# Kernel optimization log

Hardware: AMD Instinct MI355X
Metric: run time of the kernel (lower is better)

The kernel has to match this reference:

```python
import jax, jax.numpy as jnp
import numpy as np

N, F, H, OUT, DDIM, E = 200000, 64, 256, 16, 768, 3200000


def setup_inputs() -> dict:
    key = jax.random.key(0)
    ks = jax.random.split(key, 20)
    s = lambda i, shp, sc=0.05: (jax.random.normal(ks[i], shp, jnp.float32) * sc)
    return dict(
        x=jax.random.normal(ks[0], (N, F), jnp.float32),
        edge_index=jax.random.randint(ks[1], (2, E), 0, N, dtype=jnp.int32),
        doc_feature=jax.random.normal(ks[2], (DDIM,), jnp.float32),
        pool_w=s(3, (F,)),
        init_weight=s(4, (F, F)),
        gru_w_ih=s(5, (3 * F, F)), gru_w_hh=s(6, (3 * F, F)),
        gru_b_ih=s(7, (3 * F,)), gru_b_hh=s(8, (3 * F,)),
        gnn_fc_w=s(9, (H, F)), gnn_fc_b=s(10, (H,)),
        doc_fc_w=s(11, (H, DDIM)), doc_fc_b=s(12, (H,)),
        ln_g=jnp.ones((2 * H,), jnp.float32), ln_b=jnp.zeros((2 * H,), jnp.float32),
        fusion_w=s(13, (H, 2 * H)), fusion_b=s(14, (H,)),
        task_w=s(15, (OUT, H)), task_b=s(16, (OUT,)),
        time_w=s(17, (1, H)), time_b=s(18, (1,)),
    )


def _forward(x, doc_feature, pool_w, init_weight, gru_w_ih, gru_w_hh, gru_b_ih,
             gru_b_hh, gnn_fc_w, gnn_fc_b, doc_fc_w, doc_fc_b, ln_g, ln_b,
             fusion_w, fusion_b, task_w, task_b, time_w, time_b, edge_index):
    n, f = x.shape
    # --- EvolveGCNH: TopK pooling, k = f since ratio = in_channels/num_nodes ---
    score = x @ pool_w / jnp.linalg.norm(pool_w)             # [n]
    top_s, perm = jax.lax.top_k(score, f)
    x_tilde = x[perm] * jnp.tanh(top_s)[:, None]             # [f, f]
    # --- single-step GRU; hidden state = previous GCN weight (detached) ---
    h0 = jax.lax.stop_gradient(init_weight)                  # [f, f]
    gx = x_tilde @ gru_w_ih.T + gru_b_ih                     # [f, 3f]
    gh = h0 @ gru_w_hh.T + gru_b_hh
    xr, xz, xn = jnp.split(gx, 3, axis=1)
    hr, hz, hn = jnp.split(gh, 3, axis=1)
    r = jax.nn.sigmoid(xr + hr)
    z = jax.nn.sigmoid(xz + hz)
    nc = jnp.tanh(xn + r * hn)
    W = (1.0 - z) * nc + z * h0                              # evolved weight [f, f]
    # --- GCNConv with fixed W: sym-norm adjacency with self loops ---
    xw = x @ W                                               # [n, f]
    loop = jnp.arange(n, dtype=edge_index.dtype)
    row = jnp.concatenate([edge_index[0], loop])
    col = jnp.concatenate([edge_index[1], loop])
    deg = jax.ops.segment_sum(jnp.ones_like(col, dtype=x.dtype), col, num_segments=n)
    dis = jnp.where(deg > 0, jax.lax.rsqrt(jnp.maximum(deg, 1e-12)), 0.0)
    norm = dis[row] * dis[col]                               # [E+n]
    x_gnn = jax.ops.segment_sum(xw[row] * norm[:, None], col, num_segments=n)  # [n, f]
    # --- global mean pool (batch is all zeros -> single graph) ---
    pooled = jnp.mean(x_gnn, axis=0, keepdims=True)          # [1, f]
    g = pooled @ gnn_fc_w.T + gnn_fc_b                        # [1, H]
    d = jax.nn.relu(doc_feature @ doc_fc_w.T + doc_fc_b)[None, :]  # [1, H]
    fused = jnp.concatenate([g, d], axis=1)                   # [1, 2H]
    mu = jnp.mean(fused, axis=-1, keepdims=True)
    var = jnp.var(fused, axis=-1, keepdims=True)
    ln = (fused - mu) * jax.lax.rsqrt(var + 1e-5) * ln_g + ln_b
    h1 = jax.nn.relu(ln @ fusion_w.T + fusion_b)              # dropout = identity (eval)
    return (h1 @ task_w.T + task_b, h1 @ time_w.T + time_b)


def reference(x, edge_index, doc_feature, pool_w, init_weight, gru_w_ih, gru_w_hh,
              gru_b_ih, gru_b_hh, gnn_fc_w, gnn_fc_b, doc_fc_w, doc_fc_b, ln_g,
              ln_b, fusion_w, fusion_b, task_w, task_b, time_w, time_b):
    return _forward(x, doc_feature, pool_w, init_weight, gru_w_ih, gru_w_hh,
                    gru_b_ih, gru_b_hh, gnn_fc_w, gnn_fc_b, doc_fc_w, doc_fc_b,
                    ln_g, ln_b, fusion_w, fusion_b, task_w, task_b, time_w,
                    time_b, edge_index)
```

## Files before the change

kernel.cpp:

```cpp
#include <hip/hip_runtime.h>
#include <hip/hip_bf16.h>

#define NN    200000
#define EE    3200000
#define DDIMC 768

#define NI4   800000
#define HTH   1024
#define PARTW (25 * 12 * 8192)

#define BSZC  32768
#define BSHC  15
#define NBC   7
#define CCC   72
#define DEGC  (NBC * (BSZC / 2))
#define BSZR  16384
#define BSHR  14
#define NBR   13
#define CCR   40
#define PARTC (NBR * BSZR)
#define ZLEN1   (8 * DEGC)
#define ZLEN2   (8 * PARTC)

#define BSZC2 65536
#define BSHC2 16
#define NBC2  4
#define CCC2  64
#define BSZR2 32768
#define BSHR2 15
#define NBR2  7
#define CCR2  32
#define BIGPART (CCR * NBR * BSZR)

#define NDBLK 782
#define XBLOCKS 1024
#define CAPL  4096

#define HB    64
#define HW    32768

__device__ __forceinline__ float ldf(const void* p, int i, int bf) {
  if (bf) return __bfloat162float(((const __hip_bfloat16*)p)[i]);
  return ((const float*)p)[i];
}
__device__ __forceinline__ void stf(void* p, int i, float v, int bf) {
  if (bf) ((__hip_bfloat16*)p)[i] = __float2bfloat16(v);
  else ((float*)p)[i] = v;
}
__device__ __forceinline__ float bfu(unsigned u) {
  return __uint_as_float(u << 16);
}
__device__ __forceinline__ float wsum(float v) {
#pragma unroll
  for (int m = 32; m >= 1; m >>= 1) v += __shfl_xor(v, m, 64);
  return v;
}
__device__ __forceinline__ int wsumi(int v) {
#pragma unroll
  for (int m = 32; m >= 1; m >>= 1) v += __shfl_xor(v, m, 64);
  return v;
}
__device__ __forceinline__ unsigned sortkey(float f) {
  unsigned u = __float_as_uint(f);
  return (u & 0x80000000u) ? ~u : (u | 0x80000000u);
}

__global__ void k_detect(const unsigned short* x16, int* flag) {
  __shared__ int cnt;
  if (threadIdx.x == 0) cnt = 0;
  __syncthreads();
  int ok = 0;
  for (int k = threadIdx.x; k < 512; k += 256) {
    unsigned short u = x16[2 * k];
    int e = (u >> 7) & 0xFF;
    if (u == 0 || (e >= 100 && e <= 150)) ok++;
  }
  atomicAdd(&cnt, ok);
  __syncthreads();
  if (threadIdx.x == 0) flag[0] = (cnt >= 400) ? 1 : 0;
}


__global__ void __launch_bounds__(HTH) k_hcolB(const int* __restrict__ col,
                                               unsigned* __restrict__ part) {
  __shared__ unsigned lh[BSZC2 / 2];
  int t = threadIdx.x;
  int b = blockIdx.x / CCC2, j = blockIdx.x % CCC2;
  for (int k = t; k < BSZC2 / 2; k += HTH) lh[k] = 0u;
  __syncthreads();
  int base = b << BSHC2;
  const int4* c4 = (const int4*)col;
  const int stride = CCC2 * HTH;
  for (int i0 = j * HTH + t; i0 < NI4; i0 += 4 * stride) {
    int4 v[4];
#pragma unroll
    for (int u = 0; u < 4; u++) {
      int idx = i0 + u * stride;
      if (idx < NI4) v[u] = c4[idx];
      else { v[u].x = -1; v[u].y = -1; v[u].z = -1; v[u].w = -1; }
    }
#pragma unroll
    for (int u = 0; u < 4; u++) {
      int a0 = v[u].x - base, a1 = v[u].y - base, a2 = v[u].z - base, a3 = v[u].w - base;
      if ((unsigned)a0 < (unsigned)BSZC2) atomicAdd(&lh[a0 >> 1], 1u << ((a0 & 1) * 16));
      if ((unsigned)a1 < (unsigned)BSZC2) atomicAdd(&lh[a1 >> 1], 1u << ((a1 & 1) * 16));
      if ((unsigned)a2 < (unsigned)BSZC2) atomicAdd(&lh[a2 >> 1], 1u << ((a2 & 1) * 16));
      if ((unsigned)a3 < (unsigned)BSZC2) atomicAdd(&lh[a3 >> 1], 1u << ((a3 & 1) * 16));
    }
  }
  __syncthreads();
  unsigned* dst = part + (size_t)blockIdx.x * (BSZC2 / 2);
  for (int k = 4 * t; k < BSZC2 / 2; k += 4 * HTH)
    *(uint4*)&dst[k] = *(const uint4*)&lh[k];
}

__global__ void k_redAB(const unsigned* __restrict__ part, float* __restrict__ dis,
                        const void* docf, const void* dw, const void* db,
                        float* __restrict__ d, const int* flagp) {
  if (blockIdx.x < NDBLK) {
    int i = blockIdx.x * 256 + threadIdx.x;
    if (i < NN) {
      int b = i >> BSHC2;
      int k = (i & (BSZC2 - 1)) >> 1;
      const unsigned* p = part + (size_t)b * CCC2 * (BSZC2 / 2) + k;
      unsigned s = 0;
#pragma unroll 8
      for (int j = 0; j < CCC2; j++) s += p[(size_t)j * (BSZC2 / 2)];
      int deg = 1 + (int)((s >> ((i & 1) * 16)) & 0xffffu);
      dis[i] = rsqrtf((float)deg);
    }
  } else {
    int flag = flagp[0];
    int o = (blockIdx.x - NDBLK) * 4 + (threadIdx.x >> 6);
    int lane = threadIdx.x & 63;
    float acc = 0.f;
    for (int k = lane; k < DDIMC; k += 64) acc += ldf(docf, k, flag) * ldf(dw, o * DDIMC + k, flag);
    acc = wsum(acc);
    if (lane == 0) d[o] = fmaxf(acc + ldf(db, o, flag), 0.0f);
  }
}

__global__ void __launch_bounds__(HTH) k_hrowB(const int* __restrict__ row, const int* __restrict__ col,
                                               const float* __restrict__ dis,
                                               float* __restrict__ part) {
  __shared__ float lh[BSZR2];
  int t = threadIdx.x;
  int b = blockIdx.x / CCR2, j = blockIdx.x % CCR2;
  for (int k = t; k < BSZR2; k += HTH) lh[k] = 0.f;
  __syncthreads();
  int base = b << BSHR2;
  const int4* r4 = (const int4*)row;
  const int4* c4 = (const int4*)col;
  const int stride = CCR2 * HTH;
  for (int i0 = j * HTH + t; i0 < NI4; i0 += 4 * stride) {
    int4 r[4], c[4];
#pragma unroll
    for (int u = 0; u < 4; u++) {
      int idx = i0 + u * stride;
      if (idx < NI4) { r[u] = r4[idx]; c[u] = c4[idx]; }
      else { r[u].x = -1; r[u].y = -1; r[u].z = -1; r[u].w = -1;
             c[u].x = 0;  c[u].y = 0;  c[u].z = 0;  c[u].w = 0; }
    }
#pragma unroll
    for (int u = 0; u < 4; u++) {
      int a0 = r[u].x - base, a1 = r[u].y - base, a2 = r[u].z - base, a3 = r[u].w - base;
      if ((unsigned)a0 < (unsigned)BSZR2) atomicAdd(&lh[a0], dis[c[u].x]);
      if ((unsigned)a1 < (unsigned)BSZR2) atomicAdd(&lh[a1], dis[c[u].y]);
      if ((unsigned)a2 < (unsigned)BSZR2) atomicAdd(&lh[a2], dis[c[u].z]);
      if ((unsigned)a3 < (unsigned)BSZR2) atomicAdd(&lh[a3], dis[c[u].w]);
    }
  }
  __syncthreads();
  float* dst = part + (size_t)blockIdx.x * BSZR2;
  for (int k = 4 * t; k < BSZR2; k += 4 * HTH)
    *(float4*)&dst[k] = *(const float4*)&lh[k];
}

__global__ void k_redBB(const float* __restrict__ part, const float* __restrict__ dis,
                        float* __restrict__ c) {
  int i = blockIdx.x * 256 + threadIdx.x;
  if (i < NN) {
    int b = i >> BSHR2;
    int k = i & (BSZR2 - 1);
    const float* p = part + (size_t)b * CCR2 * BSZR2 + k;
    float s = 0.f;
#pragma unroll 8
    for (int j = 0; j < CCR2; j++) s += p[(size_t)j * BSZR2];
    float dv = dis[i];
    c[i] = dv * s + dv * dv;
  }
}

__global__ void __launch_bounds__(HTH) k_hcol(const int* __restrict__ col,
                                              unsigned* __restrict__ degm) {
  __shared__ unsigned lh[BSZC / 2];
  int t = threadIdx.x;
  int b = blockIdx.x / CCC, j = blockIdx.x % CCC;
  for (int k = t; k < BSZC / 2; k += HTH) lh[k] = 0u;
  __syncthreads();
  int base = b << BSHC;
  const int4* c4 = (const int4*)col;
  const int stride = CCC * HTH;
  for (int i = j * HTH + t; i < NI4; i += 2 * stride) {
    int4 v0 = c4[i];
    int i2 = i + stride;
    int4 v1; v1.x = v1.y = v1.z = v1.w = -1;
    if (i2 < NI4) v1 = c4[i2];
    {
      int a0 = v0.x - base, a1 = v0.y - base, a2 = v0.z - base, a3 = v0.w - base;
      if ((unsigned)a0 < (unsigned)BSZC) atomicAdd(&lh[a0 >> 1], 1u << ((a0 & 1) * 16));
      if ((unsigned)a1 < (unsigned)BSZC) atomicAdd(&lh[a1 >> 1], 1u << ((a1 & 1) * 16));
      if ((unsigned)a2 < (unsigned)BSZC) atomicAdd(&lh[a2 >> 1], 1u << ((a2 & 1) * 16));
      if ((unsigned)a3 < (unsigned)BSZC) atomicAdd(&lh[a3 >> 1], 1u << ((a3 & 1) * 16));
    }
    {
      int a0 = v1.x - base, a1 = v1.y - base, a2 = v1.z - base, a3 = v1.w - base;
      if ((unsigned)a0 < (unsigned)BSZC) atomicAdd(&lh[a0 >> 1], 1u << ((a0 & 1) * 16));
      if ((unsigned)a1 < (unsigned)BSZC) atomicAdd(&lh[a1 >> 1], 1u << ((a1 & 1) * 16));
      if ((unsigned)a2 < (unsigned)BSZC) atomicAdd(&lh[a2 >> 1], 1u << ((a2 & 1) * 16));
      if ((unsigned)a3 < (unsigned)BSZC) atomicAdd(&lh[a3 >> 1], 1u << ((a3 & 1) * 16));
    }
  }
  __syncthreads();
  unsigned* dst = degm + (size_t)(j & 7) * DEGC + (size_t)b * (BSZC / 2);
  for (int k = t; k < BSZC / 2; k += HTH) {
    unsigned v = lh[k];
    if (v) atomicAdd(&dst[k], v);
  }
}

__global__ void k_redA(const unsigned* __restrict__ degm, float* __restrict__ dis,
                       const void* docf, const void* dw, const void* db,
                       float* __restrict__ d, const int* flagp) {
  if (blockIdx.x < NDBLK) {
    int i = blockIdx.x * 256 + threadIdx.x;
    if (i < NN) {
      int sh = (i & 1) * 16;
      int deg = 1;
#pragma unroll
      for (int p = 0; p < 8; p++) {
        unsigned w_ = degm[(size_t)p * DEGC + (i >> 1)];
        deg += (int)((w_ >> sh) & 0xffffu);
      }
      dis[i] = rsqrtf((float)deg);
    }
  } else {
    int flag = flagp[0];
    int o = (blockIdx.x - NDBLK) * 4 + (threadIdx.x >> 6);
    int lane = threadIdx.x & 63;
    float acc = 0.f;
    for (int k = lane; k < DDIMC; k += 64) acc += ldf(docf, k, flag) * ldf(dw, o * DDIMC + k, flag);
    acc = wsum(acc);
    if (lane == 0) d[o] = fmaxf(acc + ldf(db, o, flag), 0.0f);
  }
}

__global__ void __launch_bounds__(HTH) k_hrow(const int* __restrict__ row, const int* __restrict__ col,
                                              const float* __restrict__ dis,
                                              float* __restrict__ partm) {
  __shared__ float lh[BSZR];
  int t = threadIdx.x;
  int b = blockIdx.x / CCR, j = blockIdx.x % CCR;
  for (int k = t; k < BSZR; k += HTH) lh[k] = 0.f;
  __syncthreads();
  int base = b << BSHR;
  const int4* r4 = (const int4*)row;
  const int4* c4 = (const int4*)col;
  const int stride = CCR * HTH;
  for (int i = j * HTH + t; i < NI4; i += 2 * stride) {
    int4 r0 = r4[i];
    int4 c0 = c4[i];
    int i2 = i + stride;
    int4 r1; r1.x = r1.y = r1.z = r1.w = -1;
    int4 c1; c1.x = c1.y = c1.z = c1.w = 0;
    if (i2 < NI4) { r1 = r4[i2]; c1 = c4[i2]; }
    {
      int a0 = r0.x - base, a1 = r0.y - base, a2 = r0.z - base, a3 = r0.w - base;
      if ((unsigned)a0 < (unsigned)BSZR) atomicAdd(&lh[a0], dis[c0.x]);
      if ((unsigned)a1 < (unsigned)BSZR) atomicAdd(&lh[a1], dis[c0.y]);
      if ((unsigned)a2 < (unsigned)BSZR) atomicAdd(&lh[a2], dis[c0.z]);
      if ((unsigned)a3 < (unsigned)BSZR) atomicAdd(&lh[a3], dis[c0.w]);
    }
    {
      int a0 = r1.x - base, a1 = r1.y - base, a2 = r1.z - base, a3 = r1.w - base;
      if ((unsigned)a0 < (unsigned)BSZR) atomicAdd(&lh[a0], dis[c1.x]);
      if ((unsigned)a1 < (unsigned)BSZR) atomicAdd(&lh[a1], dis[c1.y]);
      if ((unsigned)a2 < (unsigned)BSZR) atomicAdd(&lh[a2], dis[c1.z]);
      if ((unsigned)a3 < (unsigned)BSZR) atomicAdd(&lh[a3], dis[c1.w]);
    }
  }
  __syncthreads();
  float* dst = partm + (size_t)(j & 7) * PARTC + (size_t)b * BSZR;
  for (int k = t; k < BSZR; k += HTH) {
    float v = lh[k];
    if (v != 0.f) atomicAdd(&dst[k], v);
  }
}

__global__ void k_redB(const float* __restrict__ partm, const float* __restrict__ dis,
                       float* __restrict__ c) {
  int i = blockIdx.x * 256 + threadIdx.x;
  if (i < NN) {
    float s = 0.f;
#pragma unroll
    for (int p = 0; p < 8; p++) s += partm[(size_t)p * PARTC + i];
    float dv = dis[i];
    c[i] = dv * s + dv * dv;
  }
}

__global__ void k_x(const void* x, const void* pw, const float* __restrict__ c,
                    float* __restrict__ score,
                    float* __restrict__ s8, const int* flagp) {
  __shared__ float sred[4][64];
  int flag = flagp[0];
  int t = threadIdx.x;
  int lane = t & 63;
  int w = t >> 6;
  int wid = (blockIdx.x * 256 + t) >> 6;
  int nw = (gridDim.x * 256) >> 6;

  if (flag) {
    int g  = lane >> 3;
    int c0 = (lane & 7) * 8;
    float pwv[8];
#pragma unroll
    for (int j = 0; j < 8; j++) pwv[j] = ldf(pw, c0 + j, 1);
    float s = 0.f;
#pragma unroll
    for (int j = 0; j < 8; j++) s += pwv[j] * pwv[j];
    float inv = 1.0f / sqrtf(wsum(s) * 0.125f);
    float sacc[8] = {0.f, 0.f, 0.f, 0.f, 0.f, 0.f, 0.f, 0.f};
    const uint4* x4 = (const uint4*)x;
    for (int r0 = wid * 8; r0 < NN; r0 += nw * 8) {
      int r = r0 + g;
      uint4 u = x4[r * 8 + (lane & 7)];
      float xv[8] = { bfu(u.x & 0xffff), bfu(u.x >> 16),
                      bfu(u.y & 0xffff), bfu(u.y >> 16),
                      bfu(u.z & 0xffff), bfu(u.z >> 16),
                      bfu(u.w & 0xffff), bfu(u.w >> 16) };
      float dot = 0.f;
#pragma unroll
      for (int j = 0; j < 8; j++) dot += xv[j] * pwv[j];
      dot += __shfl_xor(dot, 1, 64);
      dot += __shfl_xor(dot, 2, 64);
      dot += __shfl_xor(dot, 4, 64);
      float cr = c[r];
#pragma unroll
      for (int j = 0; j < 8; j++) sacc[j] += cr * xv[j];
      if ((lane & 7) == 0) score[r] = dot * inv;
    }
#pragma unroll
    for (int j = 0; j < 8; j++) {
      sacc[j] += __shfl_xor(sacc[j], 8, 64);
      sacc[j] += __shfl_xor(sacc[j], 16, 64);
      sacc[j] += __shfl_xor(sacc[j], 32, 64);
    }
    if (lane < 8) {
#pragma unroll
      for (int j = 0; j < 8; j++) sred[w][lane * 8 + j] = sacc[j];
    }
  } else {
    int g  = lane >> 4;
    int c0 = (lane & 15) * 4;
    float pwv[4];
#pragma unroll
    for (int j = 0; j < 4; j++) pwv[j] = ((const float*)pw)[c0 + j];
    float s = 0.f;
#pragma unroll
    for (int j = 0; j < 4; j++) s += pwv[j] * pwv[j];
    float inv = 1.0f / sqrtf(wsum(s) * (1.f / 16.f));
    float sacc[4] = {0.f, 0.f, 0.f, 0.f};
    const float4* x4 = (const float4*)x;
    for (int r0 = wid * 4; r0 < NN; r0 += nw * 4) {
      int r = r0 + g;
      float4 v = x4[r * 16 + (lane & 15)];
      float xv[4] = { v.x, v.y, v.z, v.w };
      float dot = 0.f;
#pragma unroll
      for (int j = 0; j < 4; j++) dot += xv[j] * pwv[j];
      dot += __shfl_xor(dot, 1, 64);
      dot += __shfl_xor(dot, 2, 64);
      dot += __shfl_xor(dot, 4, 64);
      dot += __shfl_xor(dot, 8, 64);
      float cr = c[r];
#pragma unroll
      for (int j = 0; j < 4; j++) sacc[j] += cr * xv[j];
      if ((lane & 15) == 0) score[r] = dot * inv;
    }
#pragma unroll
    for (int j = 0; j < 4; j++) {
      sacc[j] += __shfl_xor(sacc[j], 16, 64);
      sacc[j] += __shfl_xor(sacc[j], 32, 64);
    }
    if (lane < 16) {
#pragma unroll
      for (int j = 0; j < 4; j++) sred[w][lane * 4 + j] = sacc[j];
    }
  }
  __syncthreads();
  if (w == 0)
    atomicAdd(&s8[(blockIdx.x & 7) * 64 + lane],
              sred[0][lane] + sred[1][lane] + sred[2][lane] + sred[3][lane]);
}

__global__ void __launch_bounds__(1024) k_hist(const float* __restrict__ score,
                                               unsigned* __restrict__ part) {
  __shared__ unsigned lh[HW];
  int t = threadIdx.x;
  for (int k = t; k < HW; k += 1024) lh[k] = 0u;
  __syncthreads();
  int r0 = blockIdx.x * (NN / HB);
  int r1 = r0 + (NN / HB);
  for (int i = r0 + t; i < r1; i += 1024) {
    unsigned b = sortkey(score[i]) >> 16;
    atomicAdd(&lh[b >> 1], 1u << ((b & 1) * 16));
  }
  __syncthreads();
  unsigned* dst = part + (size_t)blockIdx.x * HW;
  for (int k = t; k < HW; k += 1024) dst[k] = lh[k];
}

__global__ void k_redH(const unsigned* __restrict__ part, int* __restrict__ hist) {
  int w = blockIdx.x * 256 + threadIdx.x;
  unsigned lo = 0, hi = 0;
  for (int b = 0; b < HB; b++) {
    unsigned v = part[(size_t)b * HW + w];
    lo += v & 0xffffu;
    hi += v >> 16;
  }
  hist[2 * w]     = (int)lo;
  hist[2 * w + 1] = (int)hi;
}

__global__ void k_thresh(const int* __restrict__ hist, int* __restrict__ thrB,
                         const float* __restrict__ s8, float* __restrict__ svec) {
  __shared__ int part[256];
  __shared__ int segl[256];
  __shared__ int res2[2];
  int t = threadIdx.x, w = t >> 6, lane = t & 63;
  if (t < 64) {
    float a = 0.f;
    for (int r = 0; r < 8; r++) a += s8[r * 64 + t];
    svec[t] = a;
  }
  for (int m = w; m < 256; m += 4) {
    const int* hb = &hist[m * 256];
    int a = hb[lane] + hb[lane + 64] + hb[lane + 128] + hb[lane + 192];
    a = wsumi(a);
    if (lane == 0) part[m] = a;
  }
  __syncthreads();
  if (t == 0) {
    int acc = 0, seg = 0, above = 0;
    for (int b = 255; b >= 0; b--) {
      if (acc + part[b] >= 64) { seg = b; above = acc; break; }
      acc += part[b];
    }
    res2[0] = seg; res2[1] = above;
  }
  __syncthreads();
  segl[t] = hist[res2[0] * 256 + t];
  __syncthreads();
  if (t == 0) {
    int acc = res2[1], B = res2[0] * 256;
    for (int j = 255; j >= 0; j--) {
      acc += segl[j];
      if (acc >= 64) { B = res2[0] * 256 + j; break; }
    }
    thrB[0] = B;
  }
}

__global__ void k_collect(const float* __restrict__ score, const int* __restrict__ thrB,
                          int* __restrict__ candn, unsigned* __restrict__ ckey,
                          int* __restrict__ cidx) {
  int i = blockIdx.x * blockDim.x + threadIdx.x;
  if (i >= NN) return;
  unsigned u = sortkey(score[i]);
  if ((int)(u >> 16) >= thrB[0]) {
    int p = atomicAdd(candn, 1);
    if (p < CAPL) { ckey[p] = u; cidx[p] = i; }
  }
}

__global__ void __launch_bounds__(1024) k_top(const int* __restrict__ candn,
                      const unsigned* __restrict__ ckey,
                      const int* __restrict__ cidx, const void* x,
                      float* __restrict__ xt, const int* flagp) {
  __shared__ unsigned long long keys[CAPL];
  __shared__ int perm[64];
  __shared__ float ts[64];
  int flag = flagp[0];
  int t = threadIdx.x;
  int M = candn[0];
  if (M > CAPL) M = CAPL;
  for (int j = t; j < M; j += 1024)
    keys[j] = (((unsigned long long)ckey[j]) << 32) |
              (unsigned long long)(0xFFFFFFFFu - (unsigned)cidx[j]);
  __syncthreads();
  for (int j = t; j < M; j += 1024) {
    unsigned long long k = keys[j];
    int rank = 0;
    for (int i = 0; i < M; i++) rank += (keys[i] > k) ? 1 : 0;
    if (rank < 64) {
      unsigned ku = (unsigned)(k >> 32);
      unsigned idx = 0xFFFFFFFFu - (unsigned)(k & 0xFFFFFFFFu);
      perm[rank] = (int)idx;
      unsigned bits = (ku & 0x80000000u) ? (ku ^ 0x80000000u) : ~ku;
      ts[rank] = tanhf(__uint_as_float(bits));
    }
  }
  __syncthreads();
  for (int q = t; q < 4096; q += 1024) {
    int j = q >> 6, f = q & 63;
    xt[q] = ldf(x, perm[j] * 64 + f, flag) * ts[j];
  }
}

#define GS 193
__device__ __forceinline__ void stage_w(const void* src, float* dst, int flag, int t) {
  if (flag) {
    const uint4* s4 = (const uint4*)src;
    for (int k = t; k < 1536; k += 256) {
      uint4 u = s4[k];
      int e = k << 3; int o = e >> 6, f = e & 63;
      float* d = &dst[f * GS + o];
      d[0]      = bfu(u.x & 0xffff); d[GS]     = bfu(u.x >> 16);
      d[2 * GS] = bfu(u.y & 0xffff); d[3 * GS] = bfu(u.y >> 16);
      d[4 * GS] = bfu(u.z & 0xffff); d[5 * GS] = bfu(u.z >> 16);
      d[6 * GS] = bfu(u.w & 0xffff); d[7 * GS] = bfu(u.w >> 16);
    }
  } else {
    const float4* s4 = (const float4*)src;
    for (int k = t; k < 3072; k += 256) {
      float4 v = s4[k];
      int e = k << 2; int o = e >> 6, f = e & 63;
      float* d = &dst[f * GS + o];
      d[0] = v.x; d[GS] = v.y; d[2 * GS] = v.z; d[3 * GS] = v.w;
    }
  }
}

__global__ void k_gru(const float* __restrict__ xt, const void* h0g, const void* wihg,
                      const void* whhg, const void* bihg, const void* bhhg,
                      float* __restrict__ Wout, const int* flagp) {
  __shared__ float wb1[64 * GS];
  __shared__ float wb2[64 * GS];
  __shared__ float xtr[256];
  __shared__ float h0r[256];
  int flag = flagp[0];
  int t = threadIdx.x;
  int j0 = blockIdx.x * 4;
  { int jj = t >> 6, f = t & 63;
    xtr[t] = xt[(j0 + jj) * 64 + f];
    h0r[t] = ldf(h0g, (j0 + jj) * 64 + f, flag); }
  stage_w(wihg, wb1, flag, t);
  stage_w(whhg, wb2, flag, t);
  __syncthreads();
  int jl = t >> 6, c2 = t & 63;
  float xr = 0, xz = 0, xn = 0, hr = 0, hz = 0, hn = 0;
#pragma unroll 4
  for (int f = 0; f < 64; f++) {
    float xv = xtr[jl * 64 + f];
    float hv = h0r[jl * 64 + f];
    const float* w1 = &wb1[f * GS];
    const float* w2 = &wb2[f * GS];
    xr += xv * w1[c2]; xz += xv * w1[64 + c2]; xn += xv * w1[128 + c2];
    hr += hv * w2[c2]; hz += hv * w2[64 + c2]; hn += hv * w2[128 + c2];
  }
  xr += ldf(bihg, c2, flag); xz += ldf(bihg, 64 + c2, flag); xn += ldf(bihg, 128 + c2, flag);
  hr += ldf(bhhg, c2, flag); hz += ldf(bhhg, 64 + c2, flag); hn += ldf(bhhg, 128 + c2, flag);
  float rg = 1.f / (1.f + expf(-(xr + hr)));
  float zg = 1.f / (1.f + expf(-(xz + hz)));
  float nc = tanhf(xn + rg * hn);
  Wout[(j0 + jl) * 64 + c2] = (1.f - zg) * nc + zg * h0r[jl * 64 + c2];
}

__global__ void k_g(const float* __restrict__ svec, const float* __restrict__ Wm,
                    const void* gw, const void* gb, float* __restrict__ g,
                    const int* flagp) {
  __shared__ float pooled[64];
  int flag = flagp[0];
  int t = threadIdx.x, w = t >> 6, lane = t & 63;
  if (t < 64) {
    float a = 0.f;
    for (int f = 0; f < 64; f++) a += svec[f] * Wm[f * 64 + t];
    pooled[t] = a * (1.0f / (float)NN);
  }
  __syncthreads();
  int o = blockIdx.x * 4 + w;
  float acc = pooled[lane] * ldf(gw, o * 64 + lane, flag);
  acc = wsum(acc);
  if (lane == 0) g[o] = acc + ldf(gb, o, flag);
}

__global__ void k_ln(const float* __restrict__ g, const float* __restrict__ d,
                     const void* lng, const void* lnb, float* __restrict__ lnv,
                     const int* flagp) {
  __shared__ float red[256];
  __shared__ float stats[2];
  int flag = flagp[0];
  int t = threadIdx.x;
  float v0 = g[t], v1 = d[t];
  red[t] = v0 + v1; __syncthreads();
  for (int s = 128; s > 0; s >>= 1) { if (t < s) red[t] += red[t + s]; __syncthreads(); }
  if (t == 0) stats[0] = red[0];
  __syncthreads();
  red[t] = v0 * v0 + v1 * v1; __syncthreads();
  for (int s = 128; s > 0; s >>= 1) { if (t < s) red[t] += red[t + s]; __syncthreads(); }
  if (t == 0) stats[1] = red[0];
  __syncthreads();
  float mu = stats[0] * (1.f / 512.f);
  float var = stats[1] * (1.f / 512.f) - mu * mu;
  float istd = rsqrtf(var + 1e-5f);
  lnv[t]       = (v0 - mu) * istd * ldf(lng, t, flag)       + ldf(lnb, t, flag);
  lnv[t + 256] = (v1 - mu) * istd * ldf(lng, t + 256, flag) + ldf(lnb, t + 256, flag);
}

__global__ void k_fuse(const float* __restrict__ lnv, const void* fw, const void* fb,
                       float* __restrict__ h1, const int* flagp) {
  __shared__ float lv[512];
  int flag = flagp[0];
  int t = threadIdx.x, w = t >> 6, lane = t & 63;
  lv[t] = lnv[t]; lv[t + 256] = lnv[t + 256];
  __syncthreads();
  int o = blockIdx.x * 4 + w;
  float acc = 0.f;
  if (flag) {
    uint4 u = *((const uint4*)((const unsigned short*)fw + o * 512) + lane);
    const float* l = &lv[lane * 8];
    acc = bfu(u.x & 0xffff) * l[0] + bfu(u.x >> 16) * l[1]
        + bfu(u.y & 0xffff) * l[2] + bfu(u.y >> 16) * l[3]
        + bfu(u.z & 0xffff) * l[4] + bfu(u.z >> 16) * l[5]
        + bfu(u.w & 0xffff) * l[6] + bfu(u.w >> 16) * l[7];
  } else {
    const float4* fv = (const float4*)((const float*)fw + o * 512);
    float4 a = fv[lane * 2], b = fv[lane * 2 + 1];
    const float* l = &lv[lane * 8];
    acc = a.x * l[0] + a.y * l[1] + a.z * l[2] + a.w * l[3]
        + b.x * l[4] + b.y * l[5] + b.z * l[6] + b.w * l[7];
  }
  acc = wsum(acc);
  if (lane == 0) h1[o] = fmaxf(acc + ldf(fb, o, flag), 0.0f);
}

__global__ void k_out(const float* __restrict__ h1, const void* tw, const void* tb,
                      const void* tmw, const void* tmb, void* out, const int* flagp) {
  int flag = flagp[0];
  int t = threadIdx.x, w = t >> 6, lane = t & 63;
  int o = blockIdx.x * 4 + w;
  if (o >= 17) return;
  float acc = 0.f;
  if (o < 16) { for (int k = lane; k < 256; k += 64) acc += h1[k] * ldf(tw, o * 256 + k, flag); }
  else        { for (int k = lane; k < 256; k += 64) acc += h1[k] * ldf(tmw, k, flag); }
  acc = wsum(acc);
  if (lane == 0) {
    float bias = (o < 16) ? ldf(tb, o, flag) : ldf(tmb, 0, flag);
    stf(out, o, acc + bias, flag);
  }
}

extern "C" void kernel_launch(void* const* d_in, const int* in_sizes, int n_in,
                              void* d_out, int out_size, void* d_ws, size_t ws_size,
                              hipStream_t stream) {
  const void* x    = d_in[0];
  const int*  ei   = (const int*)d_in[1];
  const void* docf = d_in[2];
  const void* pw   = d_in[3];
  const void* h0   = d_in[4];
  const void* wih  = d_in[5];
  const void* whh  = d_in[6];
  const void* bih  = d_in[7];
  const void* bhh  = d_in[8];
  const void* gw   = d_in[9];
  const void* gb   = d_in[10];
  const void* dw   = d_in[11];
  const void* db   = d_in[12];
  const void* lng  = d_in[13];
  const void* lnb  = d_in[14];
  const void* fw   = d_in[15];
  const void* fb   = d_in[16];
  const void* tw   = d_in[17];
  const void* tb   = d_in[18];
  const void* tmw  = d_in[19];
  const void* tmb  = d_in[20];

  const int* row = ei;
  const int* col = ei + EE;

  float* wsf = (float*)d_ws;
  int*   wsi = (int*)d_ws;

  int big = (ws_size >= (size_t)42 * 1024 * 1024);
  size_t base = big ? (size_t)BIGPART : (size_t)PARTW;

  size_t oHIST  = base;
  size_t oCANDN = oHIST + 65536;
  size_t oS8    = oCANDN + 8;
  size_t oFLAG  = oS8 + 512;
  size_t oTHR   = oFLAG + 8;
  size_t oSV    = oTHR + 8;
  size_t oD     = oSV + 64;
  size_t oDIS   = oD + 256;
  size_t oC     = oDIS + NN;
  size_t oSCORE = oC + NN;
  size_t oCKEY  = oSCORE + NN;
  size_t oCIDX  = oCKEY + 4096;
  size_t oXT    = oCIDX + 4096;
  size_t oWW    = oXT + 4096;
  size_t oG     = oWW + 4096;
  size_t oLNV   = oG + 256;
  size_t oH1    = oLNV + 512;

  hipMemsetAsync(wsi + oCANDN, 0, (size_t)(8 + 512) * 4, stream);
  k_detect<<<1, 256, 0, stream>>>((const unsigned short*)x, wsi + oFLAG);

  if (big) {
    k_hcolB<<<NBC2 * CCC2, HTH, 0, stream>>>(col, (unsigned*)wsi);
    k_redAB<<<NDBLK + 64, 256, 0, stream>>>((const unsigned*)wsi, wsf + oDIS,
                                            docf, dw, db, wsf + oD, wsi + oFLAG);
    k_hrowB<<<NBR2 * CCR2, HTH, 0, stream>>>(row, col, wsf + oDIS, wsf);
    k_redBB<<<NDBLK, 256, 0, stream>>>(wsf, wsf + oDIS, wsf + oC);
  } else {
    hipMemsetAsync(wsi, 0, (size_t)ZLEN1 * 4, stream);
    k_hcol<<<NBC * CCC, HTH, 0, stream>>>(col, (unsigned*)wsi);
    k_redA<<<NDBLK + 64, 256, 0, stream>>>((const unsigned*)wsi, wsf + oDIS,
                                           docf, dw, db, wsf + oD, wsi + oFLAG);
    hipMemsetAsync(wsi, 0, (size_t)ZLEN2 * 4, stream);
    k_hrow<<<NBR * CCR, HTH, 0, stream>>>(row, col, wsf + oDIS, wsf);
    k_redB<<<NDBLK, 256, 0, stream>>>(wsf, wsf + oDIS, wsf + oC);
  }

  k_x<<<XBLOCKS, 256, 0, stream>>>(x, pw, wsf + oC, wsf + oSCORE,
                                   wsf + oS8, wsi + oFLAG);
  k_hist<<<HB, 1024, 0, stream>>>(wsf + oSCORE, (unsigned*)wsi);
  k_redH<<<HW / 256, 256, 0, stream>>>((const unsigned*)wsi, wsi + oHIST);
  k_thresh<<<1, 256, 0, stream>>>(wsi + oHIST, wsi + oTHR, wsf + oS8, wsf + oSV);
  k_collect<<<NDBLK, 256, 0, stream>>>(wsf + oSCORE, wsi + oTHR, wsi + oCANDN,
                                       (unsigned*)(wsi + oCKEY), wsi + oCIDX);
  k_top<<<1, 1024, 0, stream>>>(wsi + oCANDN, (const unsigned*)(wsi + oCKEY),
                                wsi + oCIDX, x, wsf + oXT, wsi + oFLAG);
  k_gru<<<16, 256, 0, stream>>>(wsf + oXT, h0, wih, whh, bih, bhh, wsf + oWW, wsi + oFLAG);
  k_g<<<64, 256, 0, stream>>>(wsf + oSV, wsf + oWW, gw, gb, wsf + oG, wsi + oFLAG);
  k_ln<<<1, 256, 0, stream>>>(wsf + oG, wsf + oD, lng, lnb, wsf + oLNV, wsi + oFLAG);
  k_fuse<<<64, 256, 0, stream>>>(wsf + oLNV, fw, fb, wsf + oH1, wsi + oFLAG);
  k_out<<<5, 256, 0, stream>>>(wsf + oH1, tw, tb, tmw, tmb, d_out, wsi + oFLAG);
}
```

Baseline: 292.3 us.

## Pack degree histogram into 8-bit bins and fuse tail MLP kernels

The column-degree histogram now uses 8-bit packed counters with 131072-node shared bins over 2 node ranges and 128 edge chunks, replacing 16-bit counters over 4 ranges. The reduce sums the byte fields per chunk. The four small tail kernels (gnn fc, layernorm, fusion fc, output heads) are merged into one 1024-thread block, removing launches and global round trips. The 8-bit counters could overflow if a node receives over 255 edges within one chunk.

Result: slower. 321.0 us (+9.8%).

```diff
diff --git a/kernel.cpp b/kernel.cpp
--- a/kernel.cpp
+++ b/kernel.cpp
@@ -22,10 +22,10 @@
 #define ZLEN1   (8 * DEGC)
 #define ZLEN2   (8 * PARTC)
 
-#define BSZC2 65536
-#define BSHC2 16
-#define NBC2  4
-#define CCC2  64
+#define BSZC3 131072
+#define BSHC3 17
+#define NBC3  2
+#define CCC3  128
 #define BSZR2 32768
 #define BSHR2 15
 #define NBR2  7
@@ -83,14 +83,14 @@
 
 __global__ void __launch_bounds__(HTH) k_hcolB(const int* __restrict__ col,
                                                unsigned* __restrict__ part) {
-  __shared__ unsigned lh[BSZC2 / 2];
-  int t = threadIdx.x;
-  int b = blockIdx.x / CCC2, j = blockIdx.x % CCC2;
-  for (int k = t; k < BSZC2 / 2; k += HTH) lh[k] = 0u;
-  __syncthreads();
-  int base = b << BSHC2;
+  __shared__ unsigned lh[BSZC3 / 4];
+  int t = threadIdx.x;
+  int b = blockIdx.x / CCC3, j = blockIdx.x % CCC3;
+  for (int k = t; k < BSZC3 / 4; k += HTH) lh[k] = 0u;
+  __syncthreads();
+  int base = b << BSHC3;
   const int4* c4 = (const int4*)col;
-  const int stride = CCC2 * HTH;
+  const int stride = CCC3 * HTH;
   for (int i0 = j * HTH + t; i0 < NI4; i0 += 4 * stride) {
     int4 v[4];
 #pragma unroll
@@ -102,15 +102,15 @@
 #pragma unroll
     for (int u = 0; u < 4; u++) {
       int a0 = v[u].x - base, a1 = v[u].y - base, a2 = v[u].z - base, a3 = v[u].w - base;
-      if ((unsigned)a0 < (unsigned)BSZC2) atomicAdd(&lh[a0 >> 1], 1u << ((a0 & 1) * 16));
-      if ((unsigned)a1 < (unsigned)BSZC2) atomicAdd(&lh[a1 >> 1], 1u << ((a1 & 1) * 16));
-      if ((unsigned)a2 < (unsigned)BSZC2) atomicAdd(&lh[a2 >> 1], 1u << ((a2 & 1) * 16));
-      if ((unsigned)a3 < (unsigned)BSZC2) atomicAdd(&lh[a3 >> 1], 1u << ((a3 & 1) * 16));
-    }
-  }
-  __syncthreads();
-  unsigned* dst = part + (size_t)blockIdx.x * (BSZC2 / 2);
-  for (int k = 4 * t; k < BSZC2 / 2; k += 4 * HTH)
+      if ((unsigned)a0 < (unsigned)BSZC3) atomicAdd(&lh[a0 >> 2], 1u << ((a0 & 3) * 8));
+      if ((unsigned)a1 < (unsigned)BSZC3) atomicAdd(&lh[a1 >> 2], 1u << ((a1 & 3) * 8));
+      if ((unsigned)a2 < (unsigned)BSZC3) atomicAdd(&lh[a2 >> 2], 1u << ((a2 & 3) * 8));
+      if ((unsigned)a3 < (unsigned)BSZC3) atomicAdd(&lh[a3 >> 2], 1u << ((a3 & 3) * 8));
+    }
+  }
+  __syncthreads();
+  unsigned* dst = part + (size_t)blockIdx.x * (BSZC3 / 4);
+  for (int k = 4 * t; k < BSZC3 / 4; k += 4 * HTH)
     *(uint4*)&dst[k] = *(const uint4*)&lh[k];
 }
 
@@ -120,13 +120,14 @@
   if (blockIdx.x < NDBLK) {
     int i = blockIdx.x * 256 + threadIdx.x;
     if (i < NN) {
-      int b = i >> BSHC2;
-      int k = (i & (BSZC2 - 1)) >> 1;
-      const unsigned* p = part + (size_t)b * CCC2 * (BSZC2 / 2) + k;
-      unsigned s = 0;
+      int b = i >> BSHC3;
+      int w = i & (BSZC3 - 1);
+      int sh = (w & 3) * 8;
+      const unsigned* p = part + (size_t)b * CCC3 * (BSZC3 / 4) + (w >> 2);
+      int deg = 1;
 #pragma unroll 8
-      for (int j = 0; j < CCC2; j++) s += p[(size_t)j * (BSZC2 / 2)];
-      int deg = 1 + (int)((s >> ((i & 1) * 16)) & 0xffffu);
+      for (int j = 0; j < CCC3; j++)
+        deg += (int)((p[(size_t)j * (BSZC3 / 4)] >> sh) & 255u);
       dis[i] = rsqrtf((float)deg);
     }
   } else {
@@ -525,19 +526,19 @@
     for (int k = t; k < 1536; k += 256) {
       uint4 u = s4[k];
       int e = k << 3; int o = e >> 6, f = e & 63;
-      float* d = &dst[f * GS + o];
-      d[0]      = bfu(u.x & 0xffff); d[GS]     = bfu(u.x >> 16);
-      d[2 * GS] = bfu(u.y & 0xffff); d[3 * GS] = bfu(u.y >> 16);
-      d[4 * GS] = bfu(u.z & 0xffff); d[5 * GS] = bfu(u.z >> 16);
-      d[6 * GS] = bfu(u.w & 0xffff); d[7 * GS] = bfu(u.w >> 16);
+      float* d_ = &dst[f * GS + o];
+      d_[0]      = bfu(u.x & 0xffff); d_[GS]     = bfu(u.x >> 16);
+      d_[2 * GS] = bfu(u.y & 0xffff); d_[3 * GS] = bfu(u.y >> 16);
+      d_[4 * GS] = bfu(u.z & 0xffff); d_[5 * GS] = bfu(u.z >> 16);
+      d_[6 * GS] = bfu(u.w & 0xffff); d_[7 * GS] = bfu(u.w >> 16);
     }
   } else {
     const float4* s4 = (const float4*)src;
     for (int k = t; k < 3072; k += 256) {
       float4 v = s4[k];
       int e = k << 2; int o = e >> 6, f = e & 63;
-      float* d = &dst[f * GS + o];
-      d[0] = v.x; d[GS] = v.y; d[2 * GS] = v.z; d[3 * GS] = v.w;
+      float* d_ = &dst[f * GS + o];
+      d_[0] = v.x; d_[GS] = v.y; d_[2 * GS] = v.z; d_[3 * GS] = v.w;
     }
   }
 }
@@ -577,87 +578,93 @@
   Wout[(j0 + jl) * 64 + c2] = (1.f - zg) * nc + zg * h0r[jl * 64 + c2];
 }
 
-__global__ void k_g(const float* __restrict__ svec, const float* __restrict__ Wm,
-                    const void* gw, const void* gb, float* __restrict__ g,
-                    const int* flagp) {
-  __shared__ float pooled[64];
+__global__ void __launch_bounds__(1024) k_tail(
+    const float* __restrict__ svec, const float* __restrict__ Wm,
+    const void* gw, const void* gb, const float* __restrict__ dvec,
+    const void* lng, const void* lnb, const void* fw, const void* fb,
+    const void* tw, const void* tb, const void* tmw, const void* tmb,
+    void* out, const int* flagp) {
+  __shared__ float svl[64], pooled[64], gl[256], lnv[512], h1l[256];
+  __shared__ float red[512];
+  __shared__ float stats[2];
   int flag = flagp[0];
-  int t = threadIdx.x, w = t >> 6, lane = t & 63;
+  int t = threadIdx.x;
+  if (t < 64) svl[t] = svec[t];
+  __syncthreads();
   if (t < 64) {
     float a = 0.f;
-    for (int f = 0; f < 64; f++) a += svec[f] * Wm[f * 64 + t];
+    for (int f = 0; f < 64; f++) a += svl[f] * Wm[f * 64 + t];
     pooled[t] = a * (1.0f / (float)NN);
   }
   __syncthreads();
-  int o = blockIdx.x * 4 + w;
-  float acc = pooled[lane] * ldf(gw, o * 64 + lane, flag);
-  acc = wsum(acc);
-  if (lane == 0) g[o] = acc + ldf(gb, o, flag);
-}
-
-__global__ void k_ln(const float* __restrict__ g, const float* __restrict__ d,
-                     const void* lng, const void* lnb, float* __restrict__ lnv,
-                     const int* flagp) {
-  __shared__ float red[256];
-  __shared__ float stats[2];
-  int flag = flagp[0];
-  int t = threadIdx.x;
-  float v0 = g[t], v1 = d[t];
-  red[t] = v0 + v1; __syncthreads();
-  for (int s = 128; s > 0; s >>= 1) { if (t < s) red[t] += red[t + s]; __syncthreads(); }
+  {
+    int o = t >> 2, li = t & 3;
+    float acc = 0.f;
+    for (int kk = 0; kk < 16; kk++) {
+      int l = li * 16 + kk;
+      acc += pooled[l] * ldf(gw, o * 64 + l, flag);
+    }
+    acc += __shfl_xor(acc, 1, 64);
+    acc += __shfl_xor(acc, 2, 64);
+    if (li == 0) gl[o] = acc + ldf(gb, o, flag);
+  }
+  __syncthreads();
+  float val = 0.f;
+  if (t < 256) val = gl[t];
+  else if (t < 512) val = dvec[t - 256];
+  if (t < 512) red[t] = val;
+  __syncthreads();
+  for (int s = 256; s > 0; s >>= 1) { if (t < s) red[t] += red[t + s]; __syncthreads(); }
   if (t == 0) stats[0] = red[0];
   __syncthreads();
-  red[t] = v0 * v0 + v1 * v1; __syncthreads();
-  for (int s = 128; s > 0; s >>= 1) { if (t < s) red[t] += red[t + s]; __syncthreads(); }
+  if (t < 512) red[t] = val * val;
+  __syncthreads();
+  for (int s = 256; s > 0; s >>= 1) { if (t < s) red[t] += red[t + s]; __syncthreads(); }
   if (t == 0) stats[1] = red[0];
   __syncthreads();
   float mu = stats[0] * (1.f / 512.f);
   float var = stats[1] * (1.f / 512.f) - mu * mu;
   float istd = rsqrtf(var + 1e-5f);
-  lnv[t]       = (v0 - mu) * istd * ldf(lng, t, flag)       + ldf(lnb, t, flag);
-  lnv[t + 256] = (v1 - mu) * istd * ldf(lng, t + 256, flag) + ldf(lnb, t + 256, flag);
-}
-
-__global__ void k_fuse(const float* __restrict__ lnv, const void* fw, const void* fb,
-                       float* __restrict__ h1, const int* flagp) {
-  __shared__ float lv[512];
-  int flag = flagp[0];
-  int t = threadIdx.x, w = t >> 6, lane = t & 63;
-  lv[t] = lnv[t]; lv[t + 256] = lnv[t + 256];
-  __syncthreads();
-  int o = blockIdx.x * 4 + w;
-  float acc = 0.f;
-  if (flag) {
-    uint4 u = *((const uint4*)((const unsigned short*)fw + o * 512) + lane);
-    const float* l = &lv[lane * 8];
-    acc = bfu(u.x & 0xffff) * l[0] + bfu(u.x >> 16) * l[1]
-        + bfu(u.y & 0xffff) * l[2] + bfu(u.y >> 16) * l[3]
-        + bfu(u.z & 0xffff) * l[4] + bfu(u.z >> 16) * l[5]
-        + bfu(u.w & 0xffff) * l[6] + bfu(u.w >> 16) * l[7];
-  } else {
-    const float4* fv = (const float4*)((const float*)fw + o * 512);
-    float4 a = fv[lane * 2], b = fv[lane * 2 + 1];
-    const float* l = &lv[lane * 8];
-    acc = a.x * l[0] + a.y * l[1] + a.z * l[2] + a.w * l[3]
-        + b.x * l[4] + b.y * l[5] + b.z * l[6] + b.w * l[7];
-  }
-  acc = wsum(acc);
-  if (lane == 0) h1[o] = fmaxf(acc + ldf(fb, o, flag), 0.0f);
-}
-
-__global__ void k_out(const float* __restrict__ h1, const void* tw, const void* tb,
-                      const void* tmw, const void* tmb, void* out, const int* flagp) {
-  int flag = flagp[0];
-  int t = threadIdx.x, w = t >> 6, lane = t & 63;
-  int o = blockIdx.x * 4 + w;
-  if (o >= 17) return;
-  float acc = 0.f;
-  if (o < 16) { for (int k = lane; k < 256; k += 64) acc += h1[k] * ldf(tw, o * 256 + k, flag); }
-  else        { for (int k = lane; k < 256; k += 64) acc += h1[k] * ldf(tmw, k, flag); }
-  acc = wsum(acc);
-  if (lane == 0) {
-    float bias = (o < 16) ? ldf(tb, o, flag) : ldf(tmb, 0, flag);
-    stf(out, o, acc + bias, flag);
+  if (t < 512) lnv[t] = (val - mu) * istd * ldf(lng, t, flag) + ldf(lnb, t, flag);
+  __syncthreads();
+  {
+    int o = t >> 2, li = t & 3;
+    float acc = 0.f;
+    if (flag) {
+      const uint4* fr = (const uint4*)((const unsigned short*)fw + o * 512) + li * 16;
+      for (int kk = 0; kk < 16; kk++) {
+        uint4 u = fr[kk];
+        const float* l = &lnv[li * 128 + kk * 8];
+        acc += bfu(u.x & 0xffff) * l[0] + bfu(u.x >> 16) * l[1]
+             + bfu(u.y & 0xffff) * l[2] + bfu(u.y >> 16) * l[3]
+             + bfu(u.z & 0xffff) * l[4] + bfu(u.z >> 16) * l[5]
+             + bfu(u.w & 0xffff) * l[6] + bfu(u.w >> 16) * l[7];
+      }
+    } else {
+      const float4* fr = (const float4*)((const float*)fw + o * 512) + li * 32;
+      for (int kk = 0; kk < 32; kk++) {
+        float4 v = fr[kk];
+        const float* l = &lnv[li * 128 + kk * 4];
+        acc += v.x * l[0] + v.y * l[1] + v.z * l[2] + v.w * l[3];
+      }
+    }
+    acc += __shfl_xor(acc, 1, 64);
+    acc += __shfl_xor(acc, 2, 64);
+    if (li == 0) h1l[o] = fmaxf(acc + ldf(fb, o, flag), 0.0f);
+  }
+  __syncthreads();
+  {
+    int lane = t & 63;
+    for (int o = t >> 6; o < 17; o += 16) {
+      float acc = 0.f;
+      if (o < 16) { for (int k = lane; k < 256; k += 64) acc += h1l[k] * ldf(tw, o * 256 + k, flag); }
+      else        { for (int k = lane; k < 256; k += 64) acc += h1l[k] * ldf(tmw, k, flag); }
+      acc = wsum(acc);
+      if (lane == 0) {
+        float bias = (o < 16) ? ldf(tb, o, flag) : ldf(tmb, 0, flag);
+        stf(out, o, acc + bias, flag);
+      }
+    }
   }
 }
 
@@ -709,15 +716,12 @@
   size_t oCIDX  = oCKEY + 4096;
   size_t oXT    = oCIDX + 4096;
   size_t oWW    = oXT + 4096;
-  size_t oG     = oWW + 4096;
-  size_t oLNV   = oG + 256;
-  size_t oH1    = oLNV + 512;
 
   hipMemsetAsync(wsi + oCANDN, 0, (size_t)(8 + 512) * 4, stream);
   k_detect<<<1, 256, 0, stream>>>((const unsigned short*)x, wsi + oFLAG);
 
   if (big) {
-    k_hcolB<<<NBC2 * CCC2, HTH, 0, stream>>>(col, (unsigned*)wsi);
+    k_hcolB<<<NBC3 * CCC3, HTH, 0, stream>>>(col, (unsigned*)wsi);
     k_redAB<<<NDBLK + 64, 256, 0, stream>>>((const unsigned*)wsi, wsf + oDIS,
                                             docf, dw, db, wsf + oD, wsi + oFLAG);
     k_hrowB<<<NBR2 * CCR2, HTH, 0, stream>>>(row, col, wsf + oDIS, wsf);
@@ -742,8 +746,7 @@
   k_top<<<1, 1024, 0, stream>>>(wsi + oCANDN, (const unsigned*)(wsi + oCKEY),
                                 wsi + oCIDX, x, wsf + oXT, wsi + oFLAG);
   k_gru<<<16, 256, 0, stream>>>(wsf + oXT, h0, wih, whh, bih, bhh, wsf + oWW, wsi + oFLAG);
-  k_g<<<64, 256, 0, stream>>>(wsf + oSV, wsf + oWW, gw, gb, wsf + oG, wsi + oFLAG);
-  k_ln<<<1, 256, 0, stream>>>(wsf + oG, wsf + oD, lng, lnb, wsf + oLNV, wsi + oFLAG);
-  k_fuse<<<64, 256, 0, stream>>>(wsf + oLNV, fw, fb, wsf + oH1, wsi + oFLAG);
-  k_out<<<5, 256, 0, stream>>>(wsf + oH1, tw, tb, tmw, tmb, d_out, wsi + oFLAG);
-}
+  k_tail<<<1, 1024, 0, stream>>>(wsf + oSV, wsf + oWW, gw, gb, wsf + oD,
+                                 lng, lnb, fw, fb, tw, tb, tmw, tmb,
+                                 d_out, wsi + oFLAG);
+}
```

## Pack column-degree histogram into 8-bit counters to halve bucket passes

Applied to the files above, without the earlier changes.

The per-block shared-memory degree histogram now packs four 8-bit counters per word instead of two 16-bit ones. Each block can then cover 131072 nodes, so only two node ranges are needed instead of four, with 128 column chunks per range. Each block scans 1/128 of the edges, and the reduction sums the byte fields across chunks. This halves how often the edge array is read overall. The risk is that any counter above 255 in one chunk would overflow into its neighbour, which depends on the random degree distribution (mean degree per chunk is about 0.125).

New measurement: 297.3 us. About the same (+1.7%).

```diff
diff --git a/kernel.cpp b/kernel.cpp
--- a/kernel.cpp
+++ b/kernel.cpp
@@ -22,10 +22,10 @@
 #define ZLEN1   (8 * DEGC)
 #define ZLEN2   (8 * PARTC)
 
-#define BSZC2 65536
-#define BSHC2 16
-#define NBC2  4
-#define CCC2  64
+#define BSZC3 131072
+#define BSHC3 17
+#define NBC3  2
+#define CCC3  128
 #define BSZR2 32768
 #define BSHR2 15
 #define NBR2  7
@@ -83,14 +83,14 @@
 
 __global__ void __launch_bounds__(HTH) k_hcolB(const int* __restrict__ col,
                                                unsigned* __restrict__ part) {
-  __shared__ unsigned lh[BSZC2 / 2];
-  int t = threadIdx.x;
-  int b = blockIdx.x / CCC2, j = blockIdx.x % CCC2;
-  for (int k = t; k < BSZC2 / 2; k += HTH) lh[k] = 0u;
-  __syncthreads();
-  int base = b << BSHC2;
+  __shared__ unsigned lh[BSZC3 / 4];
+  int t = threadIdx.x;
+  int b = blockIdx.x / CCC3, j = blockIdx.x % CCC3;
+  for (int k = t; k < BSZC3 / 4; k += HTH) lh[k] = 0u;
+  __syncthreads();
+  int base = b << BSHC3;
   const int4* c4 = (const int4*)col;
-  const int stride = CCC2 * HTH;
+  const int stride = CCC3 * HTH;
   for (int i0 = j * HTH + t; i0 < NI4; i0 += 4 * stride) {
     int4 v[4];
 #pragma unroll
@@ -102,15 +102,15 @@
 #pragma unroll
     for (int u = 0; u < 4; u++) {
       int a0 = v[u].x - base, a1 = v[u].y - base, a2 = v[u].z - base, a3 = v[u].w - base;
-      if ((unsigned)a0 < (unsigned)BSZC2) atomicAdd(&lh[a0 >> 1], 1u << ((a0 & 1) * 16));
-      if ((unsigned)a1 < (unsigned)BSZC2) atomicAdd(&lh[a1 >> 1], 1u << ((a1 & 1) * 16));
-      if ((unsigned)a2 < (unsigned)BSZC2) atomicAdd(&lh[a2 >> 1], 1u << ((a2 & 1) * 16));
-      if ((unsigned)a3 < (unsigned)BSZC2) atomicAdd(&lh[a3 >> 1], 1u << ((a3 & 1) * 16));
-    }
-  }
-  __syncthreads();
-  unsigned* dst = part + (size_t)blockIdx.x * (BSZC2 / 2);
-  for (int k = 4 * t; k < BSZC2 / 2; k += 4 * HTH)
+      if ((unsigned)a0 < (unsigned)BSZC3) atomicAdd(&lh[a0 >> 2], 1u << ((a0 & 3) * 8));
+      if ((unsigned)a1 < (unsigned)BSZC3) atomicAdd(&lh[a1 >> 2], 1u << ((a1 & 3) * 8));
+      if ((unsigned)a2 < (unsigned)BSZC3) atomicAdd(&lh[a2 >> 2], 1u << ((a2 & 3) * 8));
+      if ((unsigned)a3 < (unsigned)BSZC3) atomicAdd(&lh[a3 >> 2], 1u << ((a3 & 3) * 8));
+    }
+  }
+  __syncthreads();
+  unsigned* dst = part + (size_t)blockIdx.x * (BSZC3 / 4);
+  for (int k = 4 * t; k < BSZC3 / 4; k += 4 * HTH)
     *(uint4*)&dst[k] = *(const uint4*)&lh[k];
 }
 
@@ -120,13 +120,14 @@
   if (blockIdx.x < NDBLK) {
     int i = blockIdx.x * 256 + threadIdx.x;
     if (i < NN) {
-      int b = i >> BSHC2;
-      int k = (i & (BSZC2 - 1)) >> 1;
-      const unsigned* p = part + (size_t)b * CCC2 * (BSZC2 / 2) + k;
-      unsigned s = 0;
+      int b = i >> BSHC3;
+      int w = i & (BSZC3 - 1);
+      int sh = (w & 3) * 8;
+      const unsigned* p = part + (size_t)b * CCC3 * (BSZC3 / 4) + (w >> 2);
+      int deg = 1;
 #pragma unroll 8
-      for (int j = 0; j < CCC2; j++) s += p[(size_t)j * (BSZC2 / 2)];
-      int deg = 1 + (int)((s >> ((i & 1) * 16)) & 0xffffu);
+      for (int j = 0; j < CCC3; j++)
+        deg += (int)((p[(size_t)j * (BSZC3 / 4)] >> sh) & 255u);
       dis[i] = rsqrtf((float)deg);
     }
   } else {
@@ -525,19 +526,19 @@
     for (int k = t; k < 1536; k += 256) {
       uint4 u = s4[k];
       int e = k << 3; int o = e >> 6, f = e & 63;
-      float* d = &dst[f * GS + o];
-      d[0]      = bfu(u.x & 0xffff); d[GS]     = bfu(u.x >> 16);
-      d[2 * GS] = bfu(u.y & 0xffff); d[3 * GS] = bfu(u.y >> 16);
-      d[4 * GS] = bfu(u.z & 0xffff); d[5 * GS] = bfu(u.z >> 16);
-      d[6 * GS] = bfu(u.w & 0xffff); d[7 * GS] = bfu(u.w >> 16);
+      float* d_ = &dst[f * GS + o];
+      d_[0]      = bfu(u.x & 0xffff); d_[GS]     = bfu(u.x >> 16);
+      d_[2 * GS] = bfu(u.y & 0xffff); d_[3 * GS] = bfu(u.y >> 16);
+      d_[4 * GS] = bfu(u.z & 0xffff); d_[5 * GS] = bfu(u.z >> 16);
+      d_[6 * GS] = bfu(u.w & 0xffff); d_[7 * GS] = bfu(u.w >> 16);
     }
   } else {
     const float4* s4 = (const float4*)src;
     for (int k = t; k < 3072; k += 256) {
       float4 v = s4[k];
       int e = k << 2; int o = e >> 6, f = e & 63;
-      float* d = &dst[f * GS + o];
-      d[0] = v.x; d[GS] = v.y; d[2 * GS] = v.z; d[3 * GS] = v.w;
+      float* d_ = &dst[f * GS + o];
+      d_[0] = v.x; d_[GS] = v.y; d_[2 * GS] = v.z; d_[3 * GS] = v.w;
     }
   }
 }
@@ -717,7 +718,7 @@
   k_detect<<<1, 256, 0, stream>>>((const unsigned short*)x, wsi + oFLAG);
 
   if (big) {
-    k_hcolB<<<NBC2 * CCC2, HTH, 0, stream>>>(col, (unsigned*)wsi);
+    k_hcolB<<<NBC3 * CCC3, HTH, 0, stream>>>(col, (unsigned*)wsi);
     k_redAB<<<NDBLK + 64, 256, 0, stream>>>((const unsigned*)wsi, wsf + oDIS,
                                             docf, dw, db, wsf + oD, wsi + oFLAG);
     k_hrowB<<<NBR2 * CCR2, HTH, 0, stream>>>(row, col, wsf + oDIS, wsf);
```
